# Kernel optimization log

Hardware: AMD Instinct MI355X
Metric: run time of the kernel (lower is better)

## Reference

```python
import jax, jax.numpy as jnp
import numpy as np

E = 100      # embedding_dim
FS = 5       # filter_size
HS = 6       # hidden_size (conv output spatial)
D1, D2 = 10, 10  # emb_dim1, emb_dim2
RD = E * FS * FS  # relation_dim = 2500
NE = 100000  # num_entities
NR = 500     # num_relations
B = 256      # batch
EPS = 1e-5


def _bn(x, g, b, m, v, axis):
    shape = [1] * x.ndim
    shape[axis] = x.shape[axis]
    g, b, m, v = (t.reshape(shape) for t in (g, b, m, v))
    return (x - m) * jax.lax.rsqrt(v + EPS) * g + b


def setup_inputs() -> dict:
    key = jax.random.key(0)
    ks = jax.random.split(key, 24)
    def bn_params(k, n):
        k1, k2 = jax.random.split(k)
        return (jnp.ones((n,), jnp.float32),                       # gamma
                jnp.zeros((n,), jnp.float32),                      # beta
                0.1 * jax.random.normal(k1, (n,), jnp.float32),    # running mean
                jax.random.uniform(k2, (n,), jnp.float32, 0.5, 1.5))  # running var
    bn_rel = bn_params(ks[0], RD)
    bn0 = bn_params(ks[1], 1)
    bn1 = bn_params(ks[2], E)
    bn2 = bn_params(ks[3], E)
    inp = {
        'emb_e': jax.random.normal(ks[4], (NE, E), jnp.float32),
        'emb_rel': jax.random.normal(ks[5], (NR, RD), jnp.float32) * 0.1,
        'bn_rel_g': bn_rel[0], 'bn_rel_b': bn_rel[1], 'bn_rel_m': bn_rel[2], 'bn_rel_v': bn_rel[3],
        'bn0_g': bn0[0], 'bn0_b': bn0[1], 'bn0_m': bn0[2], 'bn0_v': bn0[3],
        'bn1_g': bn1[0], 'bn1_b': bn1[1], 'bn1_m': bn1[2], 'bn1_v': bn1[3],
        'fc_w': jax.random.normal(ks[6], (E * HS * HS, E), jnp.float32) / np.sqrt(E * HS * HS),
        'fc_b': jnp.zeros((E,), jnp.float32),
        'bn2_g': bn2[0], 'bn2_b': bn2[1], 'bn2_m': bn2[2], 'bn2_v': bn2[3],
        'bias': jnp.zeros((NE,), jnp.float32),
        'e1': jax.random.randint(ks[7], (B,), 0, NE),
        'rel': jax.random.randint(ks[8], (B,), 0, NR),
    }
    return inp


def reference(emb_e, emb_rel, bn_rel_g, bn_rel_b, bn_rel_m, bn_rel_v,
              bn0_g, bn0_b, bn0_m, bn0_v, bn1_g, bn1_b, bn1_m, bn1_v,
              fc_w, fc_b, bn2_g, bn2_b, bn2_m, bn2_v, bias, e1, rel):
    # entity embedding -> (B, 1, 10, 10)
    e1_emb = emb_e[e1].reshape(B, 1, D1, D2)
    # relation embedding -> per-sample conv filters
    r = emb_rel[rel]                                   # (B, 2500)
    r = _bn(r, bn_rel_g, bn_rel_b, bn_rel_m, bn_rel_v, axis=1)
    x0 = _bn(e1_emb, bn0_g, bn0_b, bn0_m, bn0_v, axis=1)
    filters = r.reshape(B, E, FS * FS)                 # (B, 100, 25)
    # per-sample dynamic-filter conv as one batched contraction over patches
    patches = jax.lax.conv_general_dilated_patches(
        x0, (FS, FS), (1, 1), 'VALID')                 # (B, 25, 6, 6)
    x = jnp.einsum('bkhw,bck->bchw', patches, filters)  # (B, 100, 6, 6)
    x = jax.nn.relu(_bn(x, bn1_g, bn1_b, bn1_m, bn1_v, axis=1))
    x = x.reshape(B, -1)                               # (B, 3600)
    x = x @ fc_w + fc_b                                # (B, 100)
    x = jax.nn.relu(_bn(x, bn2_g, bn2_b, bn2_m, bn2_v, axis=1))
    scores = x @ emb_e.T + bias                        # (B, NE)
    return jax.nn.sigmoid(scores)
```

## Files before the change

kernel.cpp:

```cpp
#include <hip/hip_runtime.h>
#include <hip/hip_bf16.h>
#include <hip/hip_fp16.h>

#define EPS 1e-5f
#define NE_ 100000
#define B_  256

typedef _Float16 half8 __attribute__((ext_vector_type(8)));
typedef float floatx16 __attribute__((ext_vector_type(16)));

#define WS_X1    0
#define WS_PART  921600
#define WS_H16   1331200

__global__ __launch_bounds__(256) void k_conv(
    const float* __restrict__ emb_e,
    const float* __restrict__ emb_rel,
    const float* __restrict__ bnr_g, const float* __restrict__ bnr_b,
    const float* __restrict__ bnr_m, const float* __restrict__ bnr_v,
    const float* __restrict__ bn0_g, const float* __restrict__ bn0_b,
    const float* __restrict__ bn0_m, const float* __restrict__ bn0_v,
    const float* __restrict__ bn1_g, const float* __restrict__ bn1_b,
    const float* __restrict__ bn1_m, const float* __restrict__ bn1_v,
    const int* __restrict__ e1, const int* __restrict__ rel,
    float* __restrict__ x1)
{
    __shared__ float x0s[100];
    __shared__ float fs[2500];

    const int b = blockIdx.x;
    const int t = threadIdx.x;
    const int ei = e1[b];
    const int ri = rel[b];

    if (t < 100) {
        float sc = bn0_g[0] * rsqrtf(bn0_v[0] + EPS);
        float sh = bn0_b[0] - bn0_m[0] * sc;
        x0s[t] = emb_e[(size_t)ei * 100 + t] * sc + sh;
    }
    for (int j = t; j < 2500; j += 256) {
        float sc = bnr_g[j] * rsqrtf(bnr_v[j] + EPS);
        fs[j] = (emb_rel[(size_t)ri * 2500 + j] - bnr_m[j]) * sc + bnr_b[j];
    }
    __syncthreads();

    for (int idx = t; idx < 3600; idx += 256) {
        int c = idx / 36;
        int p = idx - c * 36;
        int hh = p / 6, ww = p - hh * 6;
        float sum = 0.f;
        #pragma unroll
        for (int ky = 0; ky < 5; ky++) {
            #pragma unroll
            for (int kx = 0; kx < 5; kx++) {
                sum += x0s[(hh + ky) * 10 + ww + kx] * fs[c * 25 + ky * 5 + kx];
            }
        }
        float sc = bn1_g[c] * rsqrtf(bn1_v[c] + EPS);
        float y = (sum - bn1_m[c]) * sc + bn1_b[c];
        x1[(size_t)b * 3600 + idx] = fmaxf(y, 0.f);
    }
}

__global__ __launch_bounds__(256) void k_fc(
    const float* __restrict__ x1,
    const float* __restrict__ fc_w,
    float* __restrict__ partials)
{
    __shared__ float x1s[16][226];
    const int b0  = blockIdx.x * 16;
    const int ks  = blockIdx.y;
    const int kc0 = ks * 225;
    const int t = threadIdx.x;

    for (int idx = t; idx < 16 * 225; idx += 256) {
        int m = idx / 225, kk = idx - m * 225;
        x1s[m][kk] = x1[(size_t)(b0 + m) * 3600 + kc0 + kk];
    }
    __syncthreads();

    const int o  = t & 127;
    const int mg = t >> 7;
    if (o >= 100) return;

    float acc[8] = {0.f, 0.f, 0.f, 0.f, 0.f, 0.f, 0.f, 0.f};
    const float* wp = fc_w + (size_t)kc0 * 100 + o;

    for (int k0 = 0; k0 < 225; k0 += 9) {
        float wv[9];
        #pragma unroll
        for (int u = 0; u < 9; u++) wv[u] = wp[(size_t)(k0 + u) * 100];
        #pragma unroll
        for (int u = 0; u < 9; u++) {
            #pragma unroll
            for (int j = 0; j < 8; j++)
                acc[j] += x1s[mg + 2 * j][k0 + u] * wv[u];
        }
    }
    #pragma unroll
    for (int j = 0; j < 8; j++)
        partials[(size_t)ks * 25600 + (size_t)(b0 + mg + 2 * j) * 100 + o] = acc[j];
}

__global__ __launch_bounds__(256) void k_reduce(
    const float* __restrict__ partials,
    const float* __restrict__ fc_b,
    const float* __restrict__ bn2_g, const float* __restrict__ bn2_b,
    const float* __restrict__ bn2_m, const float* __restrict__ bn2_v,
    _Float16* __restrict__ h16)
{
    const int flat = blockIdx.x * 256 + threadIdx.x;
    const int b = flat / 100;
    const int o = flat - b * 100;
    float s = fc_b[o];
    #pragma unroll
    for (int ks = 0; ks < 16; ks++) s += partials[(size_t)ks * 25600 + flat];
    float sc = bn2_g[o] * rsqrtf(bn2_v[o] + EPS);
    float y = (s - bn2_m[o]) * sc + bn2_b[o];
    y = fmaxf(y, 0.f);
    h16[((o >> 3) * 256 + b) * 8 + (o & 7)] = (_Float16)y;
    if (o < 12) {
        int kp = 100 + o;
        h16[((kp >> 3) * 256 + b) * 8 + (kp & 7)] = (_Float16)0.f;
    }
}

__global__ __launch_bounds__(256) void k_scores(
    const float* __restrict__ emb_e,
    const float* __restrict__ bias,
    const _Float16* __restrict__ h16,
    float* __restrict__ out)
{
    const int t    = threadIdx.x;
    const int wave = t >> 6;
    const int lane = t & 63;
    const int l31  = lane & 31;
    const int hf   = lane >> 5;

    const int n0     = blockIdx.x * 128 + wave * 32;
    const int m_base = blockIdx.y * 128;

    const int e  = n0 + l31;
    const int el = (e < NE_) ? e : (NE_ - 1);
    const float* erow = emb_e + (size_t)el * 100;

    half8 bf[7];
    #pragma unroll
    for (int kc = 0; kc < 7; kc++) {
        const int k0 = kc * 16 + hf * 8;
        half8 h;
        if (k0 + 8 <= 100) {
            const float4 f0 = *(const float4*)(erow + k0);
            const float4 f1 = *(const float4*)(erow + k0 + 4);
            h[0] = (_Float16)f0.x; h[1] = (_Float16)f0.y;
            h[2] = (_Float16)f0.z; h[3] = (_Float16)f0.w;
            h[4] = (_Float16)f1.x; h[5] = (_Float16)f1.y;
            h[6] = (_Float16)f1.z; h[7] = (_Float16)f1.w;
        } else if (k0 < 100) {
            const float4 f0 = *(const float4*)(erow + k0);
            h[0] = (_Float16)f0.x; h[1] = (_Float16)f0.y;
            h[2] = (_Float16)f0.z; h[3] = (_Float16)f0.w;
            h[4] = (_Float16)0.f; h[5] = (_Float16)0.f;
            h[6] = (_Float16)0.f; h[7] = (_Float16)0.f;
        } else {
            #pragma unroll
            for (int j = 0; j < 8; j++) h[j] = (_Float16)0.f;
        }
        bf[kc] = h;
    }

    const half8* hA = (const half8*)h16;

    floatx16 acc[4];
    #pragma unroll
    for (int mt = 0; mt < 4; mt++)
        #pragma unroll
        for (int r = 0; r < 16; r++) acc[mt][r] = 0.f;

    #pragma unroll
    for (int mt = 0; mt < 4; mt++) {
        const int m = m_base + mt * 32 + l31;
        #pragma unroll
        for (int kc = 0; kc < 7; kc++) {
            const half8 a = hA[(kc * 2 + hf) * 256 + m];
            acc[mt] = __builtin_amdgcn_mfma_f32_32x32x16_f16(a, bf[kc], acc[mt], 0, 0, 0);
        }
    }

    if (e < NE_) {
        const float bb = bias[e];
        #pragma unroll
        for (int mt = 0; mt < 4; mt++) {
            #pragma unroll
            for (int r = 0; r < 16; r++) {
                const int row = m_base + mt * 32 + (r & 3) + 8 * (r >> 2) + 4 * hf;
                const float v = 1.f / (1.f + __expf(-(acc[mt][r] + bb)));
                out[(size_t)row * NE_ + e] = v;
            }
        }
    }
}

extern "C" void kernel_launch(void* const* d_in, const int* in_sizes, int n_in,
                              void* d_out, int out_size, void* d_ws, size_t ws_size,
                              hipStream_t stream) {
    const float* emb_e   = (const float*)d_in[0];
    const float* emb_rel = (const float*)d_in[1];
    const float* bnr_g   = (const float*)d_in[2];
    const float* bnr_b   = (const float*)d_in[3];
    const float* bnr_m   = (const float*)d_in[4];
    const float* bnr_v   = (const float*)d_in[5];
    const float* bn0_g   = (const float*)d_in[6];
    const float* bn0_b   = (const float*)d_in[7];
    const float* bn0_m   = (const float*)d_in[8];
    const float* bn0_v   = (const float*)d_in[9];
    const float* bn1_g   = (const float*)d_in[10];
    const float* bn1_b   = (const float*)d_in[11];
    const float* bn1_m   = (const float*)d_in[12];
    const float* bn1_v   = (const float*)d_in[13];
    const float* fc_w    = (const float*)d_in[14];
    const float* fc_b    = (const float*)d_in[15];
    const float* bn2_g   = (const float*)d_in[16];
    const float* bn2_b   = (const float*)d_in[17];
    const float* bn2_m   = (const float*)d_in[18];
    const float* bn2_v   = (const float*)d_in[19];
    const float* bias    = (const float*)d_in[20];
    const int* e1  = (const int*)d_in[21];
    const int* rel = (const int*)d_in[22];

    float* ws       = (float*)d_ws;
    float* x1       = ws + WS_X1;
    float* partials = ws + WS_PART;
    _Float16* h16   = (_Float16*)(ws + WS_H16);

    k_conv<<<dim3(B_), dim3(256), 0, stream>>>(
        emb_e, emb_rel,
        bnr_g, bnr_b, bnr_m, bnr_v,
        bn0_g, bn0_b, bn0_m, bn0_v,
        bn1_g, bn1_b, bn1_m, bn1_v,
        e1, rel, x1);

    k_fc<<<dim3(16, 16), dim3(256), 0, stream>>>(x1, fc_w, partials);

    k_reduce<<<dim3(100), dim3(256), 0, stream>>>(
        partials, fc_b, bn2_g, bn2_b, bn2_m, bn2_v, h16);

    k_scores<<<dim3((NE_ + 127) / 128, 2), dim3(256), 0, stream>>>(
        emb_e, bias, h16, (float*)d_out);
}
```

Measured before the change: 226.3 us.

## Fuse dynamic-filter conv into split-K FC kernel, dropping x1 round-trip

Merges the per-sample conv kernel and the split-K FC kernel into one. Each block handles 16 samples and a 5-channel slice (180 of the 3600 K values), computes that conv slice into shared memory, then multiplies it against the matching fc_w rows. This removes the global x1 intermediate and one kernel launch. In exchange, the reduce now sums 20 partial slices instead of 16, and the 16x100 entity inputs are reloaded once per K-slice block.

```diff
diff --git a/kernel.cpp b/kernel.cpp
--- a/kernel.cpp
+++ b/kernel.cpp
@@ -9,11 +9,10 @@
 typedef _Float16 half8 __attribute__((ext_vector_type(8)));
 typedef float floatx16 __attribute__((ext_vector_type(16)));
 
-#define WS_X1    0
-#define WS_PART  921600
-#define WS_H16   1331200
-
-__global__ __launch_bounds__(256) void k_conv(
+#define WS_PART  0
+#define WS_H16   512000
+
+__global__ __launch_bounds__(256) void k_convfc(
     const float* __restrict__ emb_e,
     const float* __restrict__ emb_rel,
     const float* __restrict__ bnr_g, const float* __restrict__ bnr_b,
@@ -22,60 +21,51 @@
     const float* __restrict__ bn0_m, const float* __restrict__ bn0_v,
     const float* __restrict__ bn1_g, const float* __restrict__ bn1_b,
     const float* __restrict__ bn1_m, const float* __restrict__ bn1_v,
+    const float* __restrict__ fc_w,
     const int* __restrict__ e1, const int* __restrict__ rel,
-    float* __restrict__ x1)
+    float* __restrict__ partials)
 {
-    __shared__ float x0s[100];
-    __shared__ float fs[2500];
-
-    const int b = blockIdx.x;
-    const int t = threadIdx.x;
-    const int ei = e1[b];
-    const int ri = rel[b];
-
-    if (t < 100) {
-        float sc = bn0_g[0] * rsqrtf(bn0_v[0] + EPS);
-        float sh = bn0_b[0] - bn0_m[0] * sc;
-        x0s[t] = emb_e[(size_t)ei * 100 + t] * sc + sh;
-    }
-    for (int j = t; j < 2500; j += 256) {
-        float sc = bnr_g[j] * rsqrtf(bnr_v[j] + EPS);
-        fs[j] = (emb_rel[(size_t)ri * 2500 + j] - bnr_m[j]) * sc + bnr_b[j];
+    __shared__ float x0s[16][100];
+    __shared__ float fss[16][126];
+    __shared__ float x1s[16][184];
+
+    const int bg = blockIdx.x;
+    const int ks = blockIdx.y;
+    const int c0 = ks * 5;
+    const int b0 = bg * 16;
+    const int t  = threadIdx.x;
+
+    const float sc0 = bn0_g[0] * rsqrtf(bn0_v[0] + EPS);
+    const float sh0 = bn0_b[0] - bn0_m[0] * sc0;
+
+    for (int idx = t; idx < 16 * 100; idx += 256) {
+        int s = idx / 100, j = idx - s * 100;
+        x0s[s][j] = emb_e[(size_t)e1[b0 + s] * 100 + j] * sc0 + sh0;
+    }
+    for (int idx = t; idx < 16 * 125; idx += 256) {
+        int s = idx / 125, j = idx - s * 125;
+        int g = c0 * 25 + j;
+        float sc = bnr_g[g] * rsqrtf(bnr_v[g] + EPS);
+        fss[s][j] = (emb_rel[(size_t)rel[b0 + s] * 2500 + g] - bnr_m[g]) * sc + bnr_b[g];
     }
     __syncthreads();
 
-    for (int idx = t; idx < 3600; idx += 256) {
-        int c = idx / 36;
-        int p = idx - c * 36;
+    for (int idx = t; idx < 16 * 180; idx += 256) {
+        int s = idx / 180, r = idx - s * 180;
+        int cl = r / 36, p = r - cl * 36;
         int hh = p / 6, ww = p - hh * 6;
         float sum = 0.f;
         #pragma unroll
         for (int ky = 0; ky < 5; ky++) {
             #pragma unroll
             for (int kx = 0; kx < 5; kx++) {
-                sum += x0s[(hh + ky) * 10 + ww + kx] * fs[c * 25 + ky * 5 + kx];
+                sum += x0s[s][(hh + ky) * 10 + ww + kx] * fss[s][cl * 25 + ky * 5 + kx];
             }
         }
+        int c = c0 + cl;
         float sc = bn1_g[c] * rsqrtf(bn1_v[c] + EPS);
         float y = (sum - bn1_m[c]) * sc + bn1_b[c];
-        x1[(size_t)b * 3600 + idx] = fmaxf(y, 0.f);
-    }
-}
-
-__global__ __launch_bounds__(256) void k_fc(
-    const float* __restrict__ x1,
-    const float* __restrict__ fc_w,
-    float* __restrict__ partials)
-{
-    __shared__ float x1s[16][226];
-    const int b0  = blockIdx.x * 16;
-    const int ks  = blockIdx.y;
-    const int kc0 = ks * 225;
-    const int t = threadIdx.x;
-
-    for (int idx = t; idx < 16 * 225; idx += 256) {
-        int m = idx / 225, kk = idx - m * 225;
-        x1s[m][kk] = x1[(size_t)(b0 + m) * 3600 + kc0 + kk];
+        x1s[s][r] = fmaxf(y, 0.f);
     }
     __syncthreads();
 
@@ -84,9 +74,9 @@
     if (o >= 100) return;
 
     float acc[8] = {0.f, 0.f, 0.f, 0.f, 0.f, 0.f, 0.f, 0.f};
-    const float* wp = fc_w + (size_t)kc0 * 100 + o;
-
-    for (int k0 = 0; k0 < 225; k0 += 9) {
+    const float* wp = fc_w + (size_t)(c0 * 36) * 100 + o;
+
+    for (int k0 = 0; k0 < 180; k0 += 9) {
         float wv[9];
         #pragma unroll
         for (int u = 0; u < 9; u++) wv[u] = wp[(size_t)(k0 + u) * 100];
@@ -114,7 +104,7 @@
     const int o = flat - b * 100;
     float s = fc_b[o];
     #pragma unroll
-    for (int ks = 0; ks < 16; ks++) s += partials[(size_t)ks * 25600 + flat];
+    for (int ks = 0; ks < 20; ks++) s += partials[(size_t)ks * 25600 + flat];
     float sc = bn2_g[o] * rsqrtf(bn2_v[o] + EPS);
     float y = (s - bn2_m[o]) * sc + bn2_b[o];
     y = fmaxf(y, 0.f);
@@ -229,18 +219,15 @@
     const int* rel = (const int*)d_in[22];
 
     float* ws       = (float*)d_ws;
-    float* x1       = ws + WS_X1;
     float* partials = ws + WS_PART;
     _Float16* h16   = (_Float16*)(ws + WS_H16);
 
-    k_conv<<<dim3(B_), dim3(256), 0, stream>>>(
+    k_convfc<<<dim3(16, 20), dim3(256), 0, stream>>>(
         emb_e, emb_rel,
         bnr_g, bnr_b, bnr_m, bnr_v,
         bn0_g, bn0_b, bn0_m, bn0_v,
         bn1_g, bn1_b, bn1_m, bn1_v,
-        e1, rel, x1);
-
-    k_fc<<<dim3(16, 16), dim3(256), 0, stream>>>(x1, fc_w, partials);
+        fc_w, e1, rel, partials);
 
     k_reduce<<<dim3(100), dim3(256), 0, stream>>>(
         partials, fc_b, bn2_g, bn2_b, bn2_m, bn2_v, h16);
```

After: 242.1 us. 7.0% more time.
